# Performance work log

Hardware: AMD Instinct MI355X
Metric: run time of the kernel (lower is better)

The kernel has to match this reference:

```python
import jax, jax.numpy as jnp
import numpy as np

QUERY_DIM = 1024
CONTEXT_DIM = 1024
HEADS = 8
DIM_HEAD = 64
INNER = HEADS * DIM_HEAD  # 512
SCALE = DIM_HEAD ** -0.5


def setup_inputs() -> dict:
    key = jax.random.key(0)
    ks = jax.random.split(key, 7)
    B, N, M = 2, 2048, 2048
    x = jax.random.normal(ks[0], (B, N, QUERY_DIM), dtype=jnp.float32)
    context = jax.random.normal(ks[1], (B, M, CONTEXT_DIM), dtype=jnp.float32)
    # nn.Linear weights (stored as [out, in] in torch; we use [in, out] here)
    Wq = jax.random.normal(ks[2], (QUERY_DIM, INNER), dtype=jnp.float32) * (QUERY_DIM ** -0.5)
    Wk = jax.random.normal(ks[3], (CONTEXT_DIM, INNER), dtype=jnp.float32) * (CONTEXT_DIM ** -0.5)
    Wv = jax.random.normal(ks[4], (CONTEXT_DIM, INNER), dtype=jnp.float32) * (CONTEXT_DIM ** -0.5)
    Wo = jax.random.normal(ks[5], (INNER, QUERY_DIM), dtype=jnp.float32) * (INNER ** -0.5)
    bo = jax.random.normal(ks[6], (QUERY_DIM,), dtype=jnp.float32) * 0.01
    return {"x": x, "context": context, "Wq": Wq, "Wk": Wk, "Wv": Wv, "Wo": Wo, "bo": bo}


def reference(x, context, Wq, Wk, Wv, Wo, bo):
    B, N, _ = x.shape
    M = context.shape[1]
    # projections (no bias, matching nn.Linear(bias=False))
    q = (x @ Wq).reshape(B, N, HEADS, DIM_HEAD)          # b i h d
    k = (context @ Wk).reshape(B, M, HEADS, DIM_HEAD)    # b j h d
    v = (context @ Wv).reshape(B, M, HEADS, DIM_HEAD)    # b j h d
    # scores in fp32 (ATTN_PRECISION=='fp32' path)
    sim = jnp.einsum('bihd,bjhd->bhij', q.astype(jnp.float32), k.astype(jnp.float32)) * SCALE
    attn = jax.nn.softmax(sim, axis=-1).astype(v.dtype)  # b h i j
    out = jnp.einsum('bhij,bjhd->bihd', attn, v).reshape(B, N, INNER)
    return out @ Wo + bo  # dropout p=0.0 is identity
```

## Files before the change

### kernel.cpp

```cpp
#include <hip/hip_runtime.h>
#include <math.h>

typedef __bf16 bf16_t;
typedef __bf16 bf16x8 __attribute__((ext_vector_type(8)));
typedef __bf16 bf16x4 __attribute__((ext_vector_type(4)));
typedef float  f32x4  __attribute__((ext_vector_type(4)));

#define MFMA16(a, b, c) __builtin_amdgcn_mfma_f32_16x16x32_bf16((a), (b), (c), 0, 0, 0)

#define INNER   512
#define DHEAD   64
#define QSCALE  0.18033688f

__device__ __forceinline__ void g2l(const bf16_t* g, bf16_t* l) {
  __builtin_amdgcn_global_load_lds(
      (const __attribute__((address_space(1))) unsigned int*)g,
      (__attribute__((address_space(3))) unsigned int*)l, 16, 0, 0);
}

__global__ __launch_bounds__(256) void pre_w_k(const float* __restrict__ Wq,
                                               const float* __restrict__ Wk,
                                               const float* __restrict__ Wv,
                                               const float* __restrict__ Wo,
                                               bf16_t* __restrict__ WqT,
                                               bf16_t* __restrict__ WkT,
                                               bf16_t* __restrict__ WvT,
                                               bf16_t* __restrict__ WoT) {
  __shared__ float tile[64][65];
  int t = blockIdx.x;
  int z = t >> 7, bid = t & 127;
  const float* W; bf16_t* WT; int K, N;
  if (z == 0)      { W = Wq; WT = WqT; K = 1024; N = 512; }
  else if (z == 1) { W = Wk; WT = WkT; K = 1024; N = 512; }
  else if (z == 2) { W = Wv; WT = WvT; K = 1024; N = 512; }
  else             { W = Wo; WT = WoT; K = 512;  N = 1024; }
  int tK = K >> 6;
  int kt = bid % tK, nt = bid / tK;
  int k0 = kt << 6, n0 = nt << 6;
  for (int idx = threadIdx.x; idx < 4096; idx += 256) {
    int r = idx >> 6, c = idx & 63;
    tile[r][c] = W[(size_t)(k0 + r) * N + n0 + c];
  }
  __syncthreads();
  for (int idx = threadIdx.x; idx < 4096; idx += 256) {
    int r = idx >> 6, c = idx & 63;
    WT[(size_t)(n0 + r) * K + k0 + c] = (bf16_t)tile[c][r];
  }
}

#define QKV_STEP(kc, CUR, NXT, PRC, PRF)                                         \
  {                                                                              \
    asm volatile("s_waitcnt vmcnt(8) lgkmcnt(0)" ::: "memory");                  \
    __builtin_amdgcn_s_barrier();                                                \
    __builtin_amdgcn_sched_barrier(0);                                           \
    {                                                                            \
      const int k0b = (((kc) + 1) & (KT - 1)) * 64;                              \
      _Pragma("unroll")                                                          \
      for (int p = 0; p < 4; ++p)                                                \
        g2l(gb + (size_t)(p * 8) * K + k0b, lB + (NXT) + p * 512);               \
    }                                                                            \
    {                                                                            \
      const int k0a = (((kc) + 2) & (KT - 1)) * 64;                              \
      _Pragma("unroll")                                                          \
      for (int p = 0; p < 4; ++p) {                                              \
        const float* s_ = ga + (size_t)(p * 8) * K + k0a;                        \
        PRF[2 * p]     = *(const f32x4*)s_;                                      \
        PRF[2 * p + 1] = *(const f32x4*)(s_ + 4);                                \
      }                                                                          \
    }                                                                            \
    _Pragma("unroll")                                                            \
    for (int ks = 0; ks < 2; ++ks) {                                             \
      const int phys = ((ks * 4 + quad) ^ (l16 & 7)) << 3;                       \
      bf16x8 af[4], bfr[4];                                                      \
      _Pragma("unroll")                                                          \
      for (int i = 0; i < 4; ++i)                                                \
        af[i] = *(const bf16x8*)&As[(CUR) + (mrow + i * 16 + l16) * 64 + phys];  \
      _Pragma("unroll")                                                          \
      for (int j = 0; j < 4; ++j)                                                \
        bfr[j] = *(const bf16x8*)&Bs[(CUR) + (ncol + j * 16 + l16) * 64 + phys]; \
      _Pragma("unroll")                                                          \
      for (int i = 0; i < 4; ++i)                                                \
        _Pragma("unroll")                                                        \
        for (int j = 0; j < 4; ++j)                                              \
          acc[i][j] = MFMA16(af[i], bfr[j], acc[i][j]);                          \
    }                                                                            \
    asm volatile("s_waitcnt vmcnt(12)" ::: "memory");                            \
    __builtin_amdgcn_sched_barrier(0);                                           \
    _Pragma("unroll")                                                            \
    for (int p = 0; p < 4; ++p) {                                                \
      bf16x8 h_;                                                                 \
      _Pragma("unroll")                                                          \
      for (int e = 0; e < 4; ++e) {                                              \
        h_[e]     = (bf16_t)PRC[2 * p][e];                                       \
        h_[4 + e] = (bf16_t)PRC[2 * p + 1][e];                                   \
      }                                                                          \
      *(bf16x8*)&lA[(NXT) + p * 512 + lane * 8] = h_;                            \
    }                                                                            \
  }

__device__ __forceinline__ void gemm_qkv_core(const float* __restrict__ A,
                                              const bf16_t* __restrict__ Bt,
                                              int row0, int n0,
                                              int mode, float scale,
                                              bf16_t* __restrict__ Cb) {
  constexpr int K = 1024, KT = 16;
  __shared__ bf16_t As[2 * 128 * 64];
  __shared__ bf16_t Bs[2 * 128 * 64];
  const int tid = threadIdx.x;
  const int w = tid >> 6, lane = tid & 63, quad = lane >> 4, l16 = lane & 15;
  const int sr8  = lane >> 3;
  const int slog = ((lane & 7) ^ sr8) << 3;
  const float*  ga = A  + (size_t)(row0 + w * 32 + sr8) * K + slog;
  const bf16_t* gb = Bt + (size_t)(n0   + w * 32 + sr8) * K + slog;
  bf16_t* lA = As + w * 2048;
  bf16_t* lB = Bs + w * 2048;

  f32x4 acc[4][4];
#pragma unroll
  for (int i = 0; i < 4; ++i)
#pragma unroll
    for (int j = 0; j < 4; ++j) acc[i][j] = f32x4{0.f, 0.f, 0.f, 0.f};

  f32x4 pA0[8], pA1[8];
  const int mrow = (w & 1) << 6, ncol = (w >> 1) << 6;

#pragma unroll
  for (int p = 0; p < 4; ++p) {
    const float* s = ga + (size_t)(p * 8) * K;
    f32x4 f0 = *(const f32x4*)s;
    f32x4 f1 = *(const f32x4*)(s + 4);
    bf16x8 h;
#pragma unroll
    for (int e = 0; e < 4; ++e) { h[e] = (bf16_t)f0[e]; h[4 + e] = (bf16_t)f1[e]; }
    *(bf16x8*)&lA[p * 512 + lane * 8] = h;
  }
#pragma unroll
  for (int p = 0; p < 4; ++p)
    g2l(gb + (size_t)(p * 8) * K, lB + p * 512);
#pragma unroll
  for (int p = 0; p < 4; ++p) {
    const float* s = ga + (size_t)(p * 8) * K + 64;
    pA0[2 * p]     = *(const f32x4*)s;
    pA0[2 * p + 1] = *(const f32x4*)(s + 4);
  }

  for (int kc = 0; kc < KT; kc += 2) {
    QKV_STEP(kc,     0,    8192, pA0, pA1);
    QKV_STEP(kc + 1, 8192, 0,    pA1, pA0);
  }

#pragma unroll
  for (int i = 0; i < 4; ++i) {
    int row = row0 + mrow + i * 16 + quad * 4;
#pragma unroll
    for (int j = 0; j < 4; ++j) {
      int col = n0 + ncol + j * 16 + l16;
      if (mode == 2) {
        int bb = row >> 11, key = row & 2047;
        int hh = col >> 6,  d   = col & 63;
        bf16x4 v = { (bf16_t)acc[i][j][0], (bf16_t)acc[i][j][1],
                     (bf16_t)acc[i][j][2], (bf16_t)acc[i][j][3] };
        *(bf16x4*)&Cb[((size_t)((bb * 8 + hh) * 64 + d)) * 2048 + key] = v;
      } else {
#pragma unroll
        for (int r = 0; r < 4; ++r)
          Cb[(size_t)(row + r) * 512 + col] = (bf16_t)(acc[i][j][r] * scale);
      }
    }
  }
}

template<int BM>
__device__ __forceinline__ void gemm_core(const bf16_t* __restrict__ Ab,
                                          const bf16_t* __restrict__ Bt,
                                          int K, int N, int row0, int n0,
                                          float* __restrict__ Cf,
                                          const float* __restrict__ bias) {
  constexpr int MI = BM / 32;
  __shared__ bf16_t As[2 * BM * 64];
  __shared__ bf16_t Bs[2 * 128 * 64];
  const int tid = threadIdx.x;
  const int w = tid >> 6, lane = tid & 63, quad = lane >> 4, l16 = lane & 15;

  const int sr8  = lane >> 3;
  const int slog = ((lane & 7) ^ sr8) << 3;
  const bf16_t* ga = Ab + (size_t)(row0 + w * (BM / 4) + sr8) * K + slog;
  const bf16_t* gb = Bt + (size_t)(n0   + w * 32 + sr8) * K + slog;
  bf16_t* lA = As + w * (BM / 4) * 64;
  bf16_t* lB = Bs + w * 2048;

  f32x4 acc[MI][4];
#pragma unroll
  for (int i = 0; i < MI; ++i)
#pragma unroll
    for (int j = 0; j < 4; ++j) acc[i][j] = f32x4{0.f, 0.f, 0.f, 0.f};

  const int mrow = (w & 1) * (BM / 2), ncol = (w >> 1) << 6;
  const int KT = K >> 6;

#pragma unroll
  for (int p = 0; p < MI; ++p)
    g2l(ga + (size_t)(p * 8) * K, lA + p * 512);
#pragma unroll
  for (int p = 0; p < 4; ++p)
    g2l(gb + (size_t)(p * 8) * K, lB + p * 512);

  for (int kc = 0; kc < KT; ++kc) {
    const int curA = (kc & 1) * (BM * 64), nxtA = ((kc + 1) & 1) * (BM * 64);
    const int curB = (kc & 1) * 8192,      nxtB = ((kc + 1) & 1) * 8192;
    __syncthreads();
    if (kc + 1 < KT) {
      const int k0 = (kc + 1) * 64;
#pragma unroll
      for (int p = 0; p < MI; ++p)
        g2l(ga + (size_t)(p * 8) * K + k0, lA + nxtA + p * 512);
#pragma unroll
      for (int p = 0; p < 4; ++p)
        g2l(gb + (size_t)(p * 8) * K + k0, lB + nxtB + p * 512);
    }
#pragma unroll
    for (int ks = 0; ks < 2; ++ks) {
      const int phys = ((ks * 4 + quad) ^ (l16 & 7)) << 3;
      bf16x8 af[MI], bfr[4];
#pragma unroll
      for (int i = 0; i < MI; ++i)
        af[i] = *(const bf16x8*)&As[curA + (mrow + i * 16 + l16) * 64 + phys];
#pragma unroll
      for (int j = 0; j < 4; ++j)
        bfr[j] = *(const bf16x8*)&Bs[curB + (ncol + j * 16 + l16) * 64 + phys];
#pragma unroll
      for (int i = 0; i < MI; ++i)
#pragma unroll
        for (int j = 0; j < 4; ++j)
          acc[i][j] = MFMA16(af[i], bfr[j], acc[i][j]);
    }
  }

#pragma unroll
  for (int i = 0; i < MI; ++i) {
    int row = row0 + mrow + i * 16 + quad * 4;
#pragma unroll
    for (int j = 0; j < 4; ++j) {
      int col = n0 + ncol + j * 16 + l16;
#pragma unroll
      for (int r = 0; r < 4; ++r)
        Cf[(size_t)(row + r) * N + col] = acc[i][j][r] + bias[col];
    }
  }
}

__global__ __launch_bounds__(256, 2) void gemm_qkv_k(const float* __restrict__ x,
                                                     const float* __restrict__ ctx,
                                                     const bf16_t* __restrict__ WqT,
                                                     const bf16_t* __restrict__ WkT,
                                                     const bf16_t* __restrict__ WvT,
                                                     bf16_t* __restrict__ Qb,
                                                     bf16_t* __restrict__ Kb,
                                                     bf16_t* __restrict__ Vt) {
  int bid = blockIdx.x;
  int z = bid >> 7;
  int xcd  = bid & 7;
  int slot = (bid & 127) >> 3;
  int m = (xcd << 2) | (slot >> 2);
  int n = slot & 3;
  const float* A   = (z == 0) ? x   : ctx;
  const bf16_t* Bt = (z == 0) ? WqT : (z == 1) ? WkT : WvT;
  bf16_t* C        = (z == 0) ? Qb  : (z == 1) ? Kb  : Vt;
  int mode         = (z == 2) ? 2 : 0;
  float scale      = (z == 0) ? QSCALE : 1.0f;
  gemm_qkv_core(A, Bt, m * 128, n * 128, mode, scale, C);
}

__global__ __launch_bounds__(256, 2) void gemm_out_k(const bf16_t* __restrict__ AO,
                                                     const bf16_t* __restrict__ WoT,
                                                     const float* __restrict__ bo,
                                                     float* __restrict__ out) {
  int bid = blockIdx.x;
  int xcd  = bid & 7;
  int slot = bid >> 3;
  int m = (xcd << 3) | (slot >> 3);
  int n = slot & 7;
  gemm_core<64>(AO, WoT, 512, 1024, m * 64, n * 128, out, bo);
}

__global__ __launch_bounds__(256, 2) void attn_k(const bf16_t* __restrict__ Qb,
                                                 const bf16_t* __restrict__ Kb,
                                                 const bf16_t* __restrict__ Vt,
                                                 bf16_t* __restrict__ AO) {
  const int tid = threadIdx.x;
  const int w = tid >> 6, lane = tid & 63, quad = lane >> 4, l16 = lane & 15;
  int bid = blockIdx.x;
  int xcd  = bid & 7;
  int slot = bid >> 3;
  const int qt = slot & 31;
  const int bh = (xcd << 1) | (slot >> 5);
  const int b = bh >> 3, h = bh & 7;

  __shared__ bf16_t Ks[2 * 128 * 64];
  __shared__ bf16_t Vs[64 * 128];
  __shared__ bf16_t Ps[64 * 136];

  const int qrow = b * 2048 + qt * 64 + w * 16 + l16;
  const bf16_t* qptr = Qb + (size_t)qrow * INNER + h * DHEAD;
  bf16x8 bq[2];
  bq[0] = *(const bf16x8*)(qptr + quad * 8);
  bq[1] = *(const bf16x8*)(qptr + 32 + quad * 8);

  f32x4 o[4];
#pragma unroll
  for (int dt = 0; dt < 4; ++dt) o[dt] = f32x4{0.f, 0.f, 0.f, 0.f};
  float m_s = -__builtin_inff(), l_s = 0.f;

  const bf16_t* kbase  = Kb + ((size_t)b * 2048) * INNER + h * DHEAD;
  const bf16_t* vtbase = Vt + ((size_t)bh * 64) * 2048;

  const int krow = lane >> 3;
  const int kcol = ((lane & 7) ^ (lane >> 3)) << 3;
  const int vrow = lane >> 4;

#pragma unroll
  for (int p = 0; p < 4; ++p)
    g2l(kbase + (size_t)(w * 32 + p * 8 + krow) * INNER + kcol,
        &Ks[w * 2048 + p * 512]);

  for (int kt = 0; kt < 16; ++kt) {
    const int cur = (kt & 1) * 8192, nxt = ((kt + 1) & 1) * 8192;
    __syncthreads();
    if (kt < 16 - 1) {
#pragma unroll
      for (int p = 0; p < 4; ++p)
        g2l(kbase + (size_t)((kt + 1) * 128 + w * 32 + p * 8 + krow) * INNER + kcol,
            &Ks[nxt + w * 2048 + p * 512]);
    }
#pragma unroll
    for (int p = 0; p < 4; ++p) {
      int vlog = ((lane & 15) ^ ((p * 4 + vrow) & 15)) << 3;
      g2l(vtbase + (size_t)(w * 16 + p * 4 + vrow) * 2048 + kt * 128 + vlog,
          &Vs[w * 2048 + p * 512]);
    }

    f32x4 s[8];
#pragma unroll
    for (int jt = 0; jt < 8; ++jt) s[jt] = f32x4{0.f, 0.f, 0.f, 0.f};
    __builtin_amdgcn_s_setprio(1);
#pragma unroll
    for (int jt = 0; jt < 8; ++jt) {
#pragma unroll
      for (int ks = 0; ks < 2; ++ks) {
        int phys = ((ks * 4 + quad) ^ (l16 & 7)) << 3;
        bf16x8 ak = *(const bf16x8*)&Ks[cur + (jt * 16 + l16) * 64 + phys];
        s[jt] = MFMA16(ak, bq[ks], s[jt]);
      }
    }
    __builtin_amdgcn_s_setprio(0);

    float mx = -__builtin_inff();
#pragma unroll
    for (int jt = 0; jt < 8; ++jt) {
      float a = fmaxf(fmaxf(s[jt][0], s[jt][1]), fmaxf(s[jt][2], s[jt][3]));
      mx = fmaxf(mx, a);
    }
    mx = fmaxf(mx, __shfl_xor(mx, 16, 64));
    mx = fmaxf(mx, __shfl_xor(mx, 32, 64));
    float mnew = fmaxf(m_s, mx);
    float alpha = __builtin_amdgcn_exp2f(m_s - mnew);
    float rs = 0.f;
#pragma unroll
    for (int jt = 0; jt < 8; ++jt) {
#pragma unroll
      for (int r = 0; r < 4; ++r) {
        float p = __builtin_amdgcn_exp2f(s[jt][r] - mnew);
        s[jt][r] = p;
        rs += p;
      }
    }
    rs += __shfl_xor(rs, 16, 64);
    rs += __shfl_xor(rs, 32, 64);
    l_s = l_s * alpha + rs;
    m_s = mnew;
#pragma unroll
    for (int dt = 0; dt < 4; ++dt) o[dt] *= alpha;

#pragma unroll
    for (int jt = 0; jt < 8; ++jt) {
      bf16x4 pk = { (bf16_t)s[jt][0], (bf16_t)s[jt][1],
                    (bf16_t)s[jt][2], (bf16_t)s[jt][3] };
      *(bf16x4*)&Ps[(w * 16 + l16) * 136 + jt * 16 + quad * 4] = pk;
    }

    __syncthreads();

    __builtin_amdgcn_s_setprio(1);
#pragma unroll
    for (int kc = 0; kc < 4; ++kc) {
      bf16x8 bp = *(const bf16x8*)&Ps[(w * 16 + l16) * 136 + kc * 32 + quad * 8];
#pragma unroll
      for (int dt = 0; dt < 4; ++dt) {
        int phys = ((kc * 4 + quad) ^ l16) << 3;
        bf16x8 av = *(const bf16x8*)&Vs[(dt * 16 + l16) * 128 + phys];
        o[dt] = MFMA16(av, bp, o[dt]);
      }
    }
    __builtin_amdgcn_s_setprio(0);
  }

  float inv = 1.0f / l_s;
#pragma unroll
  for (int dt = 0; dt < 4; ++dt) {
    bf16x4 ov = { (bf16_t)(o[dt][0] * inv), (bf16_t)(o[dt][1] * inv),
                  (bf16_t)(o[dt][2] * inv), (bf16_t)(o[dt][3] * inv) };
    *(bf16x4*)&Ps[(w * 16 + l16) * 136 + dt * 16 + quad * 4] = ov;
  }
  __syncthreads();
  {
    int sr = tid >> 2, sc = (tid & 3) << 4;
    int4 r0 = *(const int4*)&Ps[sr * 136 + sc];
    int4 r1 = *(const int4*)&Ps[sr * 136 + sc + 8];
    bf16_t* aout = AO + ((size_t)(b * 2048 + qt * 64 + sr)) * INNER + h * DHEAD + sc;
    *(int4*)aout       = r0;
    *(int4*)(aout + 8) = r1;
  }
}

extern "C" void kernel_launch(void* const* d_in, const int* in_sizes, int n_in,
                              void* d_out, int out_size, void* d_ws, size_t ws_size,
                              hipStream_t stream) {
  const float* x   = (const float*)d_in[0];
  const float* ctx = (const float*)d_in[1];
  const float* Wq  = (const float*)d_in[2];
  const float* Wk  = (const float*)d_in[3];
  const float* Wv  = (const float*)d_in[4];
  const float* Wo  = (const float*)d_in[5];
  const float* bo  = (const float*)d_in[6];
  float* out = (float*)d_out;

  char* ws = (char*)d_ws;
  const size_t MB = 1048576;
  bf16_t* WqT = (bf16_t*)(ws + 0 * MB);
  bf16_t* WkT = (bf16_t*)(ws + 1 * MB);
  bf16_t* WvT = (bf16_t*)(ws + 2 * MB);
  bf16_t* WoT = (bf16_t*)(ws + 3 * MB);
  bf16_t* Qb  = (bf16_t*)(ws + 4 * MB);
  bf16_t* Kb  = (bf16_t*)(ws + 8 * MB);
  bf16_t* Vt  = (bf16_t*)(ws + 12 * MB);
  bf16_t* AO  = (bf16_t*)(ws + 16 * MB);

  pre_w_k<<<512, 256, 0, stream>>>(Wq, Wk, Wv, Wo, WqT, WkT, WvT, WoT);
  gemm_qkv_k<<<384, 256, 0, stream>>>(x, ctx, WqT, WkT, WvT, Qb, Kb, Vt);
  attn_k<<<512, 256, 0, stream>>>(Qb, Kb, Vt, AO);
  gemm_out_k<<<512, 256, 0, stream>>>(AO, WoT, bo, out);
}
```

Baseline: 162.2 us.

## Split V projection into smaller tiles and refine attention load waits

The QKV GEMM kernel is templated on M-tile height. The V projection now runs as 256 blocks with 64-row tiles, up from 128 blocks with 128-row tiles, so the grid grows to 512 blocks for better load balance across CUs. Shared memory becomes an explicit buffer sized for the largest variant. In the attention kernel, the next K prefetch is issued unconditionally after the V load, and the full __syncthreads before the PV stage becomes a partial vmcnt wait plus barrier, so the K prefetch can stay in flight during PV. The trade-off is a redundant K load on the last iteration and more fragile hand-tuned waitcnt counts.

```diff
diff --git a/kernel.cpp b/kernel.cpp
--- a/kernel.cpp
+++ b/kernel.cpp
@@ -17,6 +17,8 @@
       (const __attribute__((address_space(1))) unsigned int*)g,
       (__attribute__((address_space(3))) unsigned int*)l, 16, 0, 0);
 }
+
+#define SBAR0() __builtin_amdgcn_sched_barrier(0)
 
 __global__ __launch_bounds__(256) void pre_w_k(const float* __restrict__ Wq,
                                                const float* __restrict__ Wk,
@@ -48,84 +50,89 @@
   }
 }
 
-#define QKV_STEP(kc, CUR, NXT, PRC, PRF)                                         \
+#define QKV_STEP(kc, CURA, NXTA, CURB, NXTB, PRC, PRF)                           \
   {                                                                              \
-    asm volatile("s_waitcnt vmcnt(8) lgkmcnt(0)" ::: "memory");                  \
+    asm volatile("s_waitcnt vmcnt(%c0) lgkmcnt(0)" :: "i"(2 * MI) : "memory");   \
     __builtin_amdgcn_s_barrier();                                                \
-    __builtin_amdgcn_sched_barrier(0);                                           \
+    SBAR0();                                                                     \
     {                                                                            \
       const int k0b = (((kc) + 1) & (KT - 1)) * 64;                              \
       _Pragma("unroll")                                                          \
       for (int p = 0; p < 4; ++p)                                                \
-        g2l(gb + (size_t)(p * 8) * K + k0b, lB + (NXT) + p * 512);               \
+        g2l(gb + (size_t)(p * 8) * K + k0b, lB + (NXTB) + p * 512);              \
     }                                                                            \
+    SBAR0();                \
     {                                                                            \
       const int k0a = (((kc) + 2) & (KT - 1)) * 64;                              \
       _Pragma("unroll")                                                          \
-      for (int p = 0; p < 4; ++p) {                                              \
+      for (int p = 0; p < MI; ++p) {                                             \
         const float* s_ = ga + (size_t)(p * 8) * K + k0a;                        \
         PRF[2 * p]     = *(const f32x4*)s_;                                      \
         PRF[2 * p + 1] = *(const f32x4*)(s_ + 4);                                \
       }                                                                          \
     }                                                                            \
+    SBAR0();                        \
     _Pragma("unroll")                                                            \
     for (int ks = 0; ks < 2; ++ks) {                                             \
       const int phys = ((ks * 4 + quad) ^ (l16 & 7)) << 3;                       \
-      bf16x8 af[4], bfr[4];                                                      \
-      _Pragma("unroll")                                                          \
-      for (int i = 0; i < 4; ++i)                                                \
-        af[i] = *(const bf16x8*)&As[(CUR) + (mrow + i * 16 + l16) * 64 + phys];  \
+      bf16x8 af[MI], bfr[4];                                                     \
+      _Pragma("unroll")                                                          \
+      for (int i = 0; i < MI; ++i)                                               \
+        af[i] = *(const bf16x8*)&As[(CURA) + (mrow + i * 16 + l16) * 64 + phys]; \
       _Pragma("unroll")                                                          \
       for (int j = 0; j < 4; ++j)                                                \
-        bfr[j] = *(const bf16x8*)&Bs[(CUR) + (ncol + j * 16 + l16) * 64 + phys]; \
-      _Pragma("unroll")                                                          \
-      for (int i = 0; i < 4; ++i)                                                \
+        bfr[j] = *(const bf16x8*)&Bs[(CURB) + (ncol + j * 16 + l16) * 64 + phys];\
+      _Pragma("unroll")                                                          \
+      for (int i = 0; i < MI; ++i)                                               \
         _Pragma("unroll")                                                        \
         for (int j = 0; j < 4; ++j)                                              \
           acc[i][j] = MFMA16(af[i], bfr[j], acc[i][j]);                          \
     }                                                                            \
-    asm volatile("s_waitcnt vmcnt(12)" ::: "memory");                            \
-    __builtin_amdgcn_sched_barrier(0);                                           \
+    asm volatile("s_waitcnt vmcnt(%c0)" :: "i"(2 * MI + 4) : "memory");          \
+    SBAR0();                                                                     \
     _Pragma("unroll")                                                            \
-    for (int p = 0; p < 4; ++p) {                                                \
+    for (int p = 0; p < MI; ++p) {                                               \
       bf16x8 h_;                                                                 \
       _Pragma("unroll")                                                          \
       for (int e = 0; e < 4; ++e) {                                              \
         h_[e]     = (bf16_t)PRC[2 * p][e];                                       \
         h_[4 + e] = (bf16_t)PRC[2 * p + 1][e];                                   \
       }                                                                          \
-      *(bf16x8*)&lA[(NXT) + p * 512 + lane * 8] = h_;                            \
+      *(bf16x8*)&lA[(NXTA) + p * 512 + lane * 8] = h_;                           \
     }                                                                            \
   }
 
-__device__ __forceinline__ void gemm_qkv_core(const float* __restrict__ A,
+template<int MI>
+__device__ __forceinline__ void gemm_qkv_core(bf16_t* sm,
+                                              const float* __restrict__ A,
                                               const bf16_t* __restrict__ Bt,
                                               int row0, int n0,
                                               int mode, float scale,
                                               bf16_t* __restrict__ Cb) {
   constexpr int K = 1024, KT = 16;
-  __shared__ bf16_t As[2 * 128 * 64];
-  __shared__ bf16_t Bs[2 * 128 * 64];
+  constexpr int ABUF = MI * 2048;
+  bf16_t* As = sm;
+  bf16_t* Bs = sm + 2 * ABUF;
   const int tid = threadIdx.x;
   const int w = tid >> 6, lane = tid & 63, quad = lane >> 4, l16 = lane & 15;
   const int sr8  = lane >> 3;
   const int slog = ((lane & 7) ^ sr8) << 3;
-  const float*  ga = A  + (size_t)(row0 + w * 32 + sr8) * K + slog;
+  const float*  ga = A  + (size_t)(row0 + w * (MI * 8) + sr8) * K + slog;
   const bf16_t* gb = Bt + (size_t)(n0   + w * 32 + sr8) * K + slog;
-  bf16_t* lA = As + w * 2048;
+  bf16_t* lA = As + w * MI * 512;
   bf16_t* lB = Bs + w * 2048;
 
-  f32x4 acc[4][4];
-#pragma unroll
-  for (int i = 0; i < 4; ++i)
+  f32x4 acc[MI][4];
+#pragma unroll
+  for (int i = 0; i < MI; ++i)
 #pragma unroll
     for (int j = 0; j < 4; ++j) acc[i][j] = f32x4{0.f, 0.f, 0.f, 0.f};
 
-  f32x4 pA0[8], pA1[8];
-  const int mrow = (w & 1) << 6, ncol = (w >> 1) << 6;
-
-#pragma unroll
-  for (int p = 0; p < 4; ++p) {
+  f32x4 pA0[2 * MI], pA1[2 * MI];
+  const int mrow = (w & 1) * (MI * 16), ncol = (w >> 1) << 6;
+
+#pragma unroll
+  for (int p = 0; p < MI; ++p) {
     const float* s = ga + (size_t)(p * 8) * K;
     f32x4 f0 = *(const f32x4*)s;
     f32x4 f1 = *(const f32x4*)(s + 4);
@@ -134,23 +141,26 @@
     for (int e = 0; e < 4; ++e) { h[e] = (bf16_t)f0[e]; h[4 + e] = (bf16_t)f1[e]; }
     *(bf16x8*)&lA[p * 512 + lane * 8] = h;
   }
+  SBAR0();
 #pragma unroll
   for (int p = 0; p < 4; ++p)
     g2l(gb + (size_t)(p * 8) * K, lB + p * 512);
-#pragma unroll
-  for (int p = 0; p < 4; ++p) {
+  SBAR0();
+#pragma unroll
+  for (int p = 0; p < MI; ++p) {
     const float* s = ga + (size_t)(p * 8) * K + 64;
     pA0[2 * p]     = *(const f32x4*)s;
     pA0[2 * p + 1] = *(const f32x4*)(s + 4);
   }
+  SBAR0();
 
   for (int kc = 0; kc < KT; kc += 2) {
-    QKV_STEP(kc,     0,    8192, pA0, pA1);
-    QKV_STEP(kc + 1, 8192, 0,    pA1, pA0);
-  }
-
-#pragma unroll
-  for (int i = 0; i < 4; ++i) {
+    QKV_STEP(kc,     0,    ABUF, 0,    8192, pA0, pA1);
+    QKV_STEP(kc + 1, ABUF, 0,    8192, 0,    pA1, pA0);
+  }
+
+#pragma unroll
+  for (int i = 0; i < MI; ++i) {
     int row = row0 + mrow + i * 16 + quad * 4;
 #pragma unroll
     for (int j = 0; j < 4; ++j) {
@@ -167,6 +177,36 @@
           Cb[(size_t)(row + r) * 512 + col] = (bf16_t)(acc[i][j][r] * scale);
       }
     }
+  }
+}
+
+__global__ __launch_bounds__(256, 2) void gemm_qkv_k(const float* __restrict__ x,
+                                                     const float* __restrict__ ctx,
+                                                     const bf16_t* __restrict__ WqT,
+                                                     const bf16_t* __restrict__ WkT,
+                                                     const bf16_t* __restrict__ WvT,
+                                                     bf16_t* __restrict__ Qb,
+                                                     bf16_t* __restrict__ Kb,
+                                                     bf16_t* __restrict__ Vt) {
+  __shared__ __align__(16) bf16_t smem[32768];
+  int bid = blockIdx.x;
+  if (bid < 256) {
+    int z = bid >> 7;
+    int t = bid & 127;
+    int xcd = t & 7, slot = t >> 3;
+    int m = (xcd << 2) | (slot >> 2);
+    int n = slot & 3;
+    const float* A   = (z == 0) ? x   : ctx;
+    const bf16_t* Bt = (z == 0) ? WqT : WkT;
+    bf16_t* C        = (z == 0) ? Qb  : Kb;
+    float scale      = (z == 0) ? QSCALE : 1.0f;
+    gemm_qkv_core<4>(smem, A, Bt, m * 128, n * 128, 0, scale, C);
+  } else {
+    int t = bid - 256;
+    int xcd = t & 7, slot = t >> 3;
+    int m = (xcd << 3) | (slot >> 2);
+    int n = slot & 3;
+    gemm_qkv_core<2>(smem, ctx, WvT, m * 64, n * 128, 2, 1.0f, Vt);
   }
 }
 
@@ -247,28 +287,6 @@
         Cf[(size_t)(row + r) * N + col] = acc[i][j][r] + bias[col];
     }
   }
-}
-
-__global__ __launch_bounds__(256, 2) void gemm_qkv_k(const float* __restrict__ x,
-                                                     const float* __restrict__ ctx,
-                                                     const bf16_t* __restrict__ WqT,
-                                                     const bf16_t* __restrict__ WkT,
-                                                     const bf16_t* __restrict__ WvT,
-                                                     bf16_t* __restrict__ Qb,
-                                                     bf16_t* __restrict__ Kb,
-                                                     bf16_t* __restrict__ Vt) {
-  int bid = blockIdx.x;
-  int z = bid >> 7;
-  int xcd  = bid & 7;
-  int slot = (bid & 127) >> 3;
-  int m = (xcd << 2) | (slot >> 2);
-  int n = slot & 3;
-  const float* A   = (z == 0) ? x   : ctx;
-  const bf16_t* Bt = (z == 0) ? WqT : (z == 1) ? WkT : WvT;
-  bf16_t* C        = (z == 0) ? Qb  : (z == 1) ? Kb  : Vt;
-  int mode         = (z == 2) ? 2 : 0;
-  float scale      = (z == 0) ? QSCALE : 1.0f;
-  gemm_qkv_core(A, Bt, m * 128, n * 128, mode, scale, C);
 }
 
 __global__ __launch_bounds__(256, 2) void gemm_out_k(const bf16_t* __restrict__ AO,
@@ -326,18 +344,21 @@
   for (int kt = 0; kt < 16; ++kt) {
     const int cur = (kt & 1) * 8192, nxt = ((kt + 1) & 1) * 8192;
     __syncthreads();
-    if (kt < 16 - 1) {
-#pragma unroll
-      for (int p = 0; p < 4; ++p)
-        g2l(kbase + (size_t)((kt + 1) * 128 + w * 32 + p * 8 + krow) * INNER + kcol,
-            &Ks[nxt + w * 2048 + p * 512]);
-    }
 #pragma unroll
     for (int p = 0; p < 4; ++p) {
       int vlog = ((lane & 15) ^ ((p * 4 + vrow) & 15)) << 3;
       g2l(vtbase + (size_t)(w * 16 + p * 4 + vrow) * 2048 + kt * 128 + vlog,
           &Vs[w * 2048 + p * 512]);
     }
+    SBAR0();
+    {
+      const int ktn = (kt + 1) & 15;
+#pragma unroll
+      for (int p = 0; p < 4; ++p)
+        g2l(kbase + (size_t)(ktn * 128 + w * 32 + p * 8 + krow) * INNER + kcol,
+            &Ks[nxt + w * 2048 + p * 512]);
+    }
+    SBAR0();
 
     f32x4 s[8];
 #pragma unroll
@@ -388,7 +409,9 @@
       *(bf16x4*)&Ps[(w * 16 + l16) * 136 + jt * 16 + quad * 4] = pk;
     }
 
-    __syncthreads();
+    asm volatile("s_waitcnt vmcnt(4) lgkmcnt(0)" ::: "memory");
+    __builtin_amdgcn_s_barrier();
+    SBAR0();
 
     __builtin_amdgcn_s_setprio(1);
 #pragma unroll
@@ -446,7 +469,7 @@
   bf16_t* AO  = (bf16_t*)(ws + 16 * MB);
 
   pre_w_k<<<512, 256, 0, stream>>>(Wq, Wk, Wv, Wo, WqT, WkT, WvT, WoT);
-  gemm_qkv_k<<<384, 256, 0, stream>>>(x, ctx, WqT, WkT, WvT, Qb, Kb, Vt);
+  gemm_qkv_k<<<512, 256, 0, stream>>>(x, ctx, WqT, WkT, WvT, Qb, Kb, Vt);
   attn_k<<<512, 256, 0, stream>>>(Qb, Kb, Vt, AO);
   gemm_out_k<<<512, 256, 0, stream>>>(AO, WoT, bo, out);
 }
```

After: 159.3 us. About the same (-1.8%).
